# Performance work log

Hardware: AMD Instinct MI355X
Metric: run time of the kernel (lower is better)

Reference implementation:

```python
import jax, jax.numpy as jnp
import numpy as np

NUM_HEADS = 12


def setup_inputs() -> dict:
    key = jax.random.key(0)
    ks = jax.random.split(key, 10)
    B, S, H = 4, 1024, 768
    hd = H // NUM_HEADS
    hk = hv = 64
    scale = 1.0 / np.sqrt(H)
    inp = {
        "hidden_states": jax.random.normal(ks[0], (B, S, H), dtype=jnp.float32),
        "attention_mask": jnp.ones((B, S), dtype=jnp.float32),
        "Wq": jax.random.normal(ks[1], (H, H), dtype=jnp.float32) * scale,
        "bq": jnp.zeros((H,), dtype=jnp.float32),
        "Wk": jax.random.normal(ks[2], (H, H), dtype=jnp.float32) * scale,
        "bk": jnp.zeros((H,), dtype=jnp.float32),
        "Wv": jax.random.normal(ks[3], (H, H), dtype=jnp.float32) * scale,
        "bv": jnp.zeros((H,), dtype=jnp.float32),
        "E_key": jax.random.normal(ks[4], (2 * hk + 1, hd), dtype=jnp.float32) * 0.02,
        "E_val": jax.random.normal(ks[5], (2 * hv + 1, hd), dtype=jnp.float32) * 0.02,
    }
    return inp


def reference(hidden_states, attention_mask, Wq, bq, Wk, bk, Wv, bv, E_key, E_val):
    B, S, H = hidden_states.shape
    hd = H // NUM_HEADS

    def split_heads(x):  # [B,S,H] -> [B,nh,S,hd]
        return x.reshape(B, S, NUM_HEADS, hd).transpose(0, 2, 1, 3)

    q = split_heads(hidden_states @ Wq + bq)
    k = split_heads(hidden_states @ Wk + bk)
    v = split_heads(hidden_states @ Wv + bv)

    # content scores (note: original code applies NO 1/sqrt(d) scaling)
    scores = jnp.einsum("bhid,bhjd->bhij", q, k)

    # relative key-position scores: scores_pos[i,j] = q_i . E_key[j-i+hk] (banded)
    Rk = E_key.shape[0]
    hk = (Rk - 1) // 2
    rel = jnp.arange(S)[None, :] - jnp.arange(S)[:, None] + hk  # [S,S]
    valid_k = (rel >= 0) & (rel < Rk)
    p = jnp.einsum("bhid,rd->bhir", q, E_key)  # [B,nh,S,Rk]
    rel_c = jnp.clip(rel, 0, Rk - 1)
    scores_pos = jnp.take_along_axis(p, rel_c[None, None, :, :], axis=-1)
    scores = scores + jnp.where(valid_k[None, None], scores_pos, 0.0)

    # attention mask: (1 - m) * finfo.min added to scores
    ext = (1.0 - attention_mask[:, None, None, :]) * jnp.finfo(scores.dtype).min
    probs = jax.nn.softmax(scores + ext, axis=-1)

    ctx = jnp.einsum("bhij,bhjd->bhid", probs, v)

    # relative value-position: ctx_pos[i] = sum_j probs[i,j] * E_val[j-i+hv]
    Rv = E_val.shape[0]
    hv = (Rv - 1) // 2
    j_idx = jnp.arange(S)[:, None] + jnp.arange(Rv)[None, :] - hv  # [S,Rv]
    valid_v = (j_idx >= 0) & (j_idx < S)
    j_c = jnp.clip(j_idx, 0, S - 1)
    probs_band = jnp.take_along_axis(probs, j_c[None, None, :, :], axis=-1)
    probs_band = probs_band * valid_v[None, None].astype(probs.dtype)
    ctx = ctx + jnp.einsum("bhir,rd->bhid", probs_band, E_val)

    return ctx.transpose(0, 2, 1, 3).reshape(B, S, H)
```

## Files before the change

### kernel.cpp

```cpp
#include <hip/hip_runtime.h>
#include <hip/hip_bf16.h>
#include <math.h>

#define NH 12
#define SEQ 1024
#define HD 64
#define HDIM 768
#define BSZ 4
#define RK 129
#define FMIN -3.4028234663852886e38f

typedef __attribute__((ext_vector_type(8))) short short8;
typedef __attribute__((ext_vector_type(4))) short short4v;
typedef __attribute__((ext_vector_type(8))) _Float16 f16x8;
typedef __attribute__((ext_vector_type(4))) float f32x4;

__device__ inline short f2bf(float x) {
    union { __hip_bfloat16 h; short s; } u;
    u.h = __float2bfloat16(x);
    return u.s;
}
__device__ inline float bf2f(short s) {
    union { __hip_bfloat16 h; short t; } u;
    u.t = s;
    return __bfloat162float(u.h);
}

__device__ inline void async_load16(void* lds, const void* g) {
    __builtin_amdgcn_global_load_lds(
        (const __attribute__((address_space(1))) unsigned int*)g,
        (__attribute__((address_space(3))) unsigned int*)lds, 16, 0, 0);
}

#define BAR()    asm volatile("s_barrier" ::: "memory")
#define WAITV0() asm volatile("s_waitcnt vmcnt(0)" ::: "memory")

#define NXCHUNK 393216
#define NECHUNK 1032
#define NEVCHUNK 1280
#define NCONVB ((NXCHUNK + NECHUNK + NEVCHUNK + 255) / 256)
#define NTRB   (144 * 3)
__global__ __launch_bounds__(256) void prep_kernel(
    const float* __restrict__ X, const float* __restrict__ Ek,
    const float* __restrict__ Ev,
    const float* __restrict__ Wq, const float* __restrict__ Wk, const float* __restrict__ Wv,
    _Float16* __restrict__ Xh, _Float16* __restrict__ Ekh, short* __restrict__ Evt,
    _Float16* __restrict__ Wtq, _Float16* __restrict__ Wtk, _Float16* __restrict__ Wtv)
{
    const int bidg = blockIdx.x;
    if (bidg < NCONVB) {
        int idx = bidg * 256 + threadIdx.x;
        if (idx < NXCHUNK + NECHUNK) {
            const float* src;
            _Float16* dst;
            if (idx < NXCHUNK) { src = X; dst = Xh; }
            else { idx -= NXCHUNK; src = Ek; dst = Ekh; }
            float4 a = ((const float4*)src)[idx * 2];
            float4 b = ((const float4*)src)[idx * 2 + 1];
            f16x8 o;
            o[0] = (_Float16)a.x; o[1] = (_Float16)a.y; o[2] = (_Float16)a.z; o[3] = (_Float16)a.w;
            o[4] = (_Float16)b.x; o[5] = (_Float16)b.y; o[6] = (_Float16)b.z; o[7] = (_Float16)b.w;
            ((f16x8*)dst)[idx] = o;
        } else if (idx < NXCHUNK + NECHUNK + NEVCHUNK) {
            idx -= NXCHUNK + NECHUNK;
            const int dim = idx / 20;
            const int r0  = (idx % 20) * 8;
            short8 o;
#pragma unroll
            for (int e = 0; e < 8; ++e) {
                int rel = r0 + e;
                float v = (rel < RK) ? Ev[(size_t)rel * HD + dim] : 0.0f;
                o[e] = f2bf(v);
            }
            *(short8*)&Evt[(size_t)dim * 160 + r0] = o;
        }
        return;
    }
    const int bid2 = bidg - NCONVB;
    const int z = bid2 / 144;
    const int r = bid2 % 144;
    const float* __restrict__ W = (z == 0) ? Wq : (z == 1) ? Wk : Wv;
    _Float16* __restrict__ Wt   = (z == 0) ? Wtq : (z == 1) ? Wtk : Wtv;

    __shared__ float sT[64][65];
    const int t  = threadIdx.x;
    const int k0 = (r / 12) * 64;
    const int n0 = (r % 12) * 64;

    const int c  = (t & 15) * 4;
    const int kr = t >> 4;
#pragma unroll
    for (int rr = 0; rr < 4; ++rr) {
        float4 v = *(const float4*)&W[(size_t)(k0 + kr + rr * 16) * HDIM + n0 + c];
        sT[c + 0][kr + rr * 16] = v.x;
        sT[c + 1][kr + rr * 16] = v.y;
        sT[c + 2][kr + rr * 16] = v.z;
        sT[c + 3][kr + rr * 16] = v.w;
    }
    __syncthreads();
    const int rn = t >> 2;
    const int ck = (t & 3) * 16;
#pragma unroll
    for (int g = 0; g < 2; ++g) {
        f16x8 o;
#pragma unroll
        for (int e = 0; e < 8; ++e) o[e] = (_Float16)sT[rn][ck + g * 8 + e];
        *(f16x8*)&Wt[(size_t)(n0 + rn) * HDIM + k0 + ck + g * 8] = o;
    }
}

__global__ __launch_bounds__(256) void qkv_mfma_kernel(
    const _Float16* __restrict__ Xh,
    const _Float16* __restrict__ Wtq, const _Float16* __restrict__ Wtk, const _Float16* __restrict__ Wtv,
    const float* __restrict__ bq, const float* __restrict__ bk, const float* __restrict__ bv,
    _Float16* __restrict__ Qo, _Float16* __restrict__ Ko, short* __restrict__ Vt)
{
    int bid = blockIdx.x;
    bid = (bid & 7) * 72 + (bid >> 3);
    const int which = bid / 192;
    const int rem   = bid % 192;
    const int n0    = (rem / 32) * 128;
    const int m0    = (rem % 32) * 128;
    const _Float16* __restrict__ Wt = (which == 0) ? Wtq : (which == 1) ? Wtk : Wtv;
    const float* __restrict__ bias  = (which == 0) ? bq : (which == 1) ? bk : bv;

    __shared__ __align__(16) _Float16 sA[128 * 64];
    __shared__ __align__(16) _Float16 sB[128 * 64];

    const int t  = threadIdx.x;
    const int w  = t >> 6, l = t & 63;
    const int lq = l & 15, lg = l >> 4;
    const int wr = w >> 1, wc = w & 1;

    f32x4 acc[4][4];
#pragma unroll
    for (int i = 0; i < 4; ++i)
#pragma unroll
        for (int j = 0; j < 4; ++j) acc[i][j] = (f32x4){0.f, 0.f, 0.f, 0.f};

    for (int k0 = 0; k0 < HDIM; k0 += 64) {
        __syncthreads();
#pragma unroll
        for (int r = 0; r < 4; ++r) {
            const int cib = r * 256 + w * 64;
            const int ci  = cib + l;
            const int row = ci >> 3, cr = ci & 7;
            const int lc  = cr ^ (row & 7);
            async_load16(&sA[(size_t)cib * 8],
                         &Xh[(size_t)(m0 + row) * HDIM + k0 + lc * 8]);
            async_load16(&sB[(size_t)cib * 8],
                         &Wt[(size_t)(n0 + row) * HDIM + k0 + lc * 8]);
        }
        __syncthreads();

        f16x8 af[4][2], bf[4][2];
#pragma unroll
        for (int i = 0; i < 4; ++i) {
#pragma unroll
            for (int ks = 0; ks < 2; ++ks) {
                int ra = wr * 64 + i * 16 + lq;
                af[i][ks] = *(const f16x8*)((const char*)sA +
                            ra * 128 + ((ks * 64 + lg * 16) ^ ((ra & 7) << 4)));
                int rb = wc * 64 + i * 16 + lq;
                bf[i][ks] = *(const f16x8*)((const char*)sB +
                            rb * 128 + ((ks * 64 + lg * 16) ^ ((rb & 7) << 4)));
            }
        }
#pragma unroll
        for (int i = 0; i < 4; ++i)
#pragma unroll
            for (int j = 0; j < 4; ++j) {
                acc[i][j] = __builtin_amdgcn_mfma_f32_16x16x32_f16(af[i][0], bf[j][0], acc[i][j], 0, 0, 0);
                acc[i][j] = __builtin_amdgcn_mfma_f32_16x16x32_f16(af[i][1], bf[j][1], acc[i][j], 0, 0, 0);
            }
    }

    _Float16* __restrict__ Yh = (which == 0) ? Qo : Ko;
#pragma unroll
    for (int i = 0; i < 4; ++i) {
        const int mb = m0 + wr * 64 + i * 16 + lg * 4;
        const int bb = mb >> 10, ss = mb & 1023;
#pragma unroll
        for (int j = 0; j < 4; ++j) {
            const int n  = n0 + wc * 64 + j * 16 + lq;
            const float bv4 = bias[n];
            const int hh = n >> 6, dd = n & 63;
            if (which == 2) {
                short4v pk;
#pragma unroll
                for (int reg = 0; reg < 4; ++reg)
                    pk[reg] = f2bf(acc[i][j][reg] + bv4);
                *(short4v*)&Vt[((size_t)(bb * NH + hh) * HD + dd) * SEQ + ss] = pk;
            } else {
#pragma unroll
                for (int reg = 0; reg < 4; ++reg) {
                    const size_t off = ((size_t)(bb * NH + hh) * SEQ + ss + reg) * HD + dd;
                    Yh[off] = (_Float16)(acc[i][j][reg] + bv4);
                }
            }
        }
    }
}

__global__ __launch_bounds__(256, 2) void attn_mfma_kernel(
    const _Float16* __restrict__ Q, const _Float16* __restrict__ K,
    const short* __restrict__ Vt, const float* __restrict__ mask,
    const _Float16* __restrict__ Ekh, const short* __restrict__ Evt,
    float* __restrict__ out)
{
    __shared__ __align__(16) _Float16 sK[2][64][64];
    __shared__ __align__(16) short    sVT[2][64][64];
    __shared__ __align__(16) short    sPscr[4][16][64];
    __shared__ __align__(16) _Float16 sPpos[4][16][129];
    __shared__ __align__(16) short    sBand[4][16][160];
    __shared__ __align__(16) short    sMask[1024];

    int bid = blockIdx.x;
    bid = (bid & 7) * 96 + (bid >> 3);
    const int bh = bid >> 4;
    const int i0 = (bid & 15) * 64;
    const int b  = bh / NH;
    const int h  = bh - b * NH;

    const int t  = threadIdx.x;
    const int w  = t >> 6;
    const int l  = t & 63;
    const int lq = l & 15;
    const int lg = l >> 4;
    const int wrow0 = i0 + w * 16;

    {
        short8 z8 = {0, 0, 0, 0, 0, 0, 0, 0};
        short8* p = (short8*)&sBand[w][0][0];
        for (int idx = l; idx < 320; idx += 64) p[idx] = z8;
    }
#pragma unroll
    for (int r = 0; r < 2; ++r) {
        const int ci = r * 256 + w * 64 + l;
        const int row = ci >> 3;
        const int lc  = (ci & 7) ^ (row & 7);
        async_load16((char*)sK + ci * 16,
                     K + ((size_t)bh * SEQ + row) * HD + lc * 8);
        async_load16((char*)sVT + ci * 16,
                     Vt + ((size_t)bh * HD + row) * SEQ + lc * 8);
    }

    const _Float16* qp = Q + ((size_t)bh * SEQ + wrow0 + lq) * HD;
    f16x8 qf0 = *(const f16x8*)&qp[lg * 8];
    f16x8 qf1 = *(const f16x8*)&qp[32 + lg * 8];

#pragma unroll
    for (int nt = 0; nt < 9; ++nt) {
        int cc = nt * 16 + lq;
        f16x8 eb0 = {0, 0, 0, 0, 0, 0, 0, 0};
        f16x8 eb1 = {0, 0, 0, 0, 0, 0, 0, 0};
        if (cc < RK) {
            eb0 = *(const f16x8*)&Ekh[(size_t)cc * HD + lg * 8];
            eb1 = *(const f16x8*)&Ekh[(size_t)cc * HD + 32 + lg * 8];
        }
        f32x4 pc = {0.f, 0.f, 0.f, 0.f};
        pc = __builtin_amdgcn_mfma_f32_16x16x32_f16(qf0, eb0, pc, 0, 0, 0);
        pc = __builtin_amdgcn_mfma_f32_16x16x32_f16(qf1, eb1, pc, 0, 0, 0);
        if (cc < RK) {
#pragma unroll
            for (int reg = 0; reg < 4; ++reg)
                sPpos[w][lg * 4 + reg][cc] = (_Float16)pc[reg];
        }
    }

    {
        float4 mv = *(const float4*)&mask[(size_t)b * SEQ + t * 4];
        short4v mo;
        mo[0] = f2bf((1.0f - mv.x) * FMIN);
        mo[1] = f2bf((1.0f - mv.y) * FMIN);
        mo[2] = f2bf((1.0f - mv.z) * FMIN);
        mo[3] = f2bf((1.0f - mv.w) * FMIN);
        *(short4v*)&sMask[t * 4] = mo;
    }

    asm volatile("s_waitcnt vmcnt(0) lgkmcnt(0)" ::: "memory");
    BAR();

    f32x4 acc[4];
#pragma unroll
    for (int nt = 0; nt < 4; ++nt) acc[nt] = (f32x4){0.f, 0.f, 0.f, 0.f};
    float lacc[4] = {0.f, 0.f, 0.f, 0.f};

    const int ck0 = lg ^ (lq & 7);
    const int ck1 = (4 + lg) ^ (lq & 7);
    short* sPw = &sPscr[w][0][0];

    for (int jt = 0; jt < 16; ++jt) {
        const int cur = jt & 1;
        const int j0  = jt * 64;

        if (jt < 15) {
            const int jn0 = j0 + 64;
#pragma unroll
            for (int r = 0; r < 2; ++r) {
                const int ci = r * 256 + w * 64 + l;
                const int row = ci >> 3;
                const int lc  = (ci & 7) ^ (row & 7);
                async_load16((char*)sK + (cur ^ 1) * 8192 + ci * 16,
                             K + ((size_t)bh * SEQ + jn0 + row) * HD + lc * 8);
                async_load16((char*)sVT + (cur ^ 1) * 8192 + ci * 16,
                             Vt + ((size_t)bh * HD + row) * SEQ + jn0 + lc * 8);
            }
        }

        const char* sKc = (const char*)sK + cur * 8192;
        f32x4 sc[4];
#pragma unroll
        for (int ct = 0; ct < 4; ++ct) {
            const int rb = (ct * 16 + lq) * 128;
            f16x8 kb0 = *(const f16x8*)(sKc + rb + ck0 * 16);
            f16x8 kb1 = *(const f16x8*)(sKc + rb + ck1 * 16);
            f32x4 s = {0.f, 0.f, 0.f, 0.f};
            s = __builtin_amdgcn_mfma_f32_16x16x32_f16(qf0, kb0, s, 0, 0, 0);
            s = __builtin_amdgcn_mfma_f32_16x16x32_f16(qf1, kb1, s, 0, 0, 0);
            sc[ct] = s;
        }

        float mt[4];
#pragma unroll
        for (int ct = 0; ct < 4; ++ct) mt[ct] = bf2f(sMask[j0 + ct * 16 + lq]);

        const bool band_active = (j0 >= wrow0 - 127) && (j0 <= wrow0 + 79);
        if (band_active) {
#pragma unroll
            for (int ct = 0; ct < 4; ++ct) {
                const int relb = j0 + ct * 16 + lq - wrow0 - lg * 4 + 64;
#pragma unroll
                for (int reg = 0; reg < 4; ++reg) {
                    const int row = lg * 4 + reg;
                    const int rel = relb - reg;
                    float s = sc[ct][reg] + mt[ct];
                    const bool inb = ((unsigned)rel < (unsigned)RK);
                    if (inb) s += (float)sPpos[w][row][rel];
                    const float p = __expf(s);
                    lacc[reg] += p;
                    const short pb = f2bf(p);
                    sPw[row * 64 + ((ct * 16 + lq) ^ ((row & 7) << 3))] = pb;
                    if (inb) sBand[w][row][rel] = pb;
                }
            }
        } else {
#pragma unroll
            for (int ct = 0; ct < 4; ++ct) {
#pragma unroll
                for (int reg = 0; reg < 4; ++reg) {
                    const int row = lg * 4 + reg;
                    const float p = __expf(sc[ct][reg] + mt[ct]);
                    lacc[reg] += p;
                    sPw[row * 64 + ((ct * 16 + lq) ^ ((row & 7) << 3))] = f2bf(p);
                }
            }
        }

        short8 pa0 = *(const short8*)((const char*)sPw + lq * 128 + ck0 * 16);
        short8 pa1 = *(const short8*)((const char*)sPw + lq * 128 + ck1 * 16);
        const char* sVc = (const char*)sVT + cur * 8192;
#pragma unroll
        for (int nt = 0; nt < 4; ++nt) {
            const int rb = (nt * 16 + lq) * 128;
            short8 vb0 = *(const short8*)(sVc + rb + ck0 * 16);
            short8 vb1 = *(const short8*)(sVc + rb + ck1 * 16);
            acc[nt] = __builtin_amdgcn_mfma_f32_16x16x32_bf16(pa0, vb0, acc[nt], 0, 0, 0);
            acc[nt] = __builtin_amdgcn_mfma_f32_16x16x32_bf16(pa1, vb1, acc[nt], 0, 0, 0);
        }

        WAITV0();
        BAR();
    }

    float linv[4];
#pragma unroll
    for (int reg = 0; reg < 4; ++reg) {
        float lr = lacc[reg];
        lr += __shfl_xor(lr, 1);
        lr += __shfl_xor(lr, 2);
        lr += __shfl_xor(lr, 4);
        lr += __shfl_xor(lr, 8);
        linv[reg] = 1.0f / lr;
    }

    short8 bandA[5];
#pragma unroll
    for (int ks = 0; ks < 5; ++ks)
        bandA[ks] = *(const short8*)&sBand[w][lq][ks * 32 + lg * 8];
#pragma unroll
    for (int nt = 0; nt < 4; ++nt) {
#pragma unroll
        for (int ks = 0; ks < 5; ++ks) {
            short8 eb = *(const short8*)&Evt[(size_t)(nt * 16 + lq) * 160 + ks * 32 + lg * 8];
            acc[nt] = __builtin_amdgcn_mfma_f32_16x16x32_bf16(bandA[ks], eb, acc[nt], 0, 0, 0);
        }
    }

#pragma unroll
    for (int nt = 0; nt < 4; ++nt) {
#pragma unroll
        for (int reg = 0; reg < 4; ++reg) {
            int qi = wrow0 + lg * 4 + reg;
            out[((size_t)b * SEQ + qi) * HDIM + h * HD + nt * 16 + lq] =
                acc[nt][reg] * linv[reg];
        }
    }
}

extern "C" void kernel_launch(void* const* d_in, const int* in_sizes, int n_in,
                              void* d_out, int out_size, void* d_ws, size_t ws_size,
                              hipStream_t stream) {
    const float* X    = (const float*)d_in[0];
    const float* mask = (const float*)d_in[1];
    const float* Wq   = (const float*)d_in[2];
    const float* bq   = (const float*)d_in[3];
    const float* Wk   = (const float*)d_in[4];
    const float* bk   = (const float*)d_in[5];
    const float* Wv   = (const float*)d_in[6];
    const float* bv   = (const float*)d_in[7];
    const float* Ek   = (const float*)d_in[8];
    const float* Ev   = (const float*)d_in[9];
    float* out        = (float*)d_out;

    char* ws = (char*)d_ws;
    const size_t SZ_QKV = (size_t)BSZ * NH * SEQ * HD * 2;
    const size_t SZ_W   = (size_t)HDIM * HDIM * 2;
    _Float16* Qh  = (_Float16*)(ws);
    _Float16* Kh  = (_Float16*)(ws + SZ_QKV);
    short*    Vt  = (short*)   (ws + 2 * SZ_QKV);
    _Float16* Xh  = (_Float16*)(ws + 3 * SZ_QKV);
    _Float16* Wtq = (_Float16*)(ws + 4 * SZ_QKV);
    _Float16* Wtk = (_Float16*)(ws + 4 * SZ_QKV + SZ_W);
    _Float16* Wtv = (_Float16*)(ws + 4 * SZ_QKV + 2 * SZ_W);
    _Float16* Ekh = (_Float16*)(ws + 4 * SZ_QKV + 3 * SZ_W);
    short*    Evt = (short*)   (ws + 4 * SZ_QKV + 3 * SZ_W + 20480);

    prep_kernel<<<NCONVB + NTRB, 256, 0, stream>>>(
        X, Ek, Ev, Wq, Wk, Wv, Xh, Ekh, Evt, Wtq, Wtk, Wtv);
    qkv_mfma_kernel<<<576, 256, 0, stream>>>(Xh, Wtq, Wtk, Wtv, bq, bk, bv, Qh, Kh, Vt);
    attn_mfma_kernel<<<768, 256, 0, stream>>>(Qh, Kh, Vt, mask, Ekh, Evt, out);
}
```

Baseline: 88.98 us.

## Fold attention mask into V and compute softmax denominator via MFMA

The additive mask is turned into a multiplicative factor exp(mask), which is applied to V in the QKV epilogue and to the band probabilities. The row sum of exp(scores) is computed by an extra MFMA against the mask-factor vector instead of per-element accumulation and shuffle reductions. The QK MFMA operands are swapped so each lane holds a transposed score tile, which allows packed 32-bit stores of P to LDS. This removes per-element mask adds and the scalar denominator accumulation, but masked positions now become 0 times exp(score) rather than an exp underflow, which can overflow or give NaN if a score is large.

```diff
diff --git a/kernel.cpp b/kernel.cpp
--- a/kernel.cpp
+++ b/kernel.cpp
@@ -113,6 +113,7 @@
     const _Float16* __restrict__ Xh,
     const _Float16* __restrict__ Wtq, const _Float16* __restrict__ Wtk, const _Float16* __restrict__ Wtv,
     const float* __restrict__ bq, const float* __restrict__ bk, const float* __restrict__ bv,
+    const float* __restrict__ maskg,
     _Float16* __restrict__ Qo, _Float16* __restrict__ Ko, short* __restrict__ Vt)
 {
     int bid = blockIdx.x;
@@ -180,6 +181,14 @@
     for (int i = 0; i < 4; ++i) {
         const int mb = m0 + wr * 64 + i * 16 + lg * 4;
         const int bb = mb >> 10, ss = mb & 1023;
+        float zz[4] = {1.f, 1.f, 1.f, 1.f};
+        if (which == 2) {
+            float4 mv = *(const float4*)&maskg[(size_t)bb * SEQ + ss];
+            zz[0] = __expf((1.0f - mv.x) * FMIN);
+            zz[1] = __expf((1.0f - mv.y) * FMIN);
+            zz[2] = __expf((1.0f - mv.z) * FMIN);
+            zz[3] = __expf((1.0f - mv.w) * FMIN);
+        }
 #pragma unroll
         for (int j = 0; j < 4; ++j) {
             const int n  = n0 + wc * 64 + j * 16 + lq;
@@ -189,7 +198,7 @@
                 short4v pk;
 #pragma unroll
                 for (int reg = 0; reg < 4; ++reg)
-                    pk[reg] = f2bf(acc[i][j][reg] + bv4);
+                    pk[reg] = f2bf((acc[i][j][reg] + bv4) * zz[reg]);
                 *(short4v*)&Vt[((size_t)(bb * NH + hh) * HD + dd) * SEQ + ss] = pk;
             } else {
 #pragma unroll
@@ -213,7 +222,7 @@
     __shared__ __align__(16) short    sPscr[4][16][64];
     __shared__ __align__(16) _Float16 sPpos[4][16][129];
     __shared__ __align__(16) short    sBand[4][16][160];
-    __shared__ __align__(16) short    sMask[1024];
+    __shared__ __align__(16) short    sZ[1024];
 
     int bid = blockIdx.x;
     bid = (bid & 7) * 96 + (bid >> 3);
@@ -270,12 +279,12 @@
 
     {
         float4 mv = *(const float4*)&mask[(size_t)b * SEQ + t * 4];
-        short4v mo;
-        mo[0] = f2bf((1.0f - mv.x) * FMIN);
-        mo[1] = f2bf((1.0f - mv.y) * FMIN);
-        mo[2] = f2bf((1.0f - mv.z) * FMIN);
-        mo[3] = f2bf((1.0f - mv.w) * FMIN);
-        *(short4v*)&sMask[t * 4] = mo;
+        short4v zo;
+        zo[0] = f2bf(__expf((1.0f - mv.x) * FMIN));
+        zo[1] = f2bf(__expf((1.0f - mv.y) * FMIN));
+        zo[2] = f2bf(__expf((1.0f - mv.z) * FMIN));
+        zo[3] = f2bf(__expf((1.0f - mv.w) * FMIN));
+        *(short4v*)&sZ[t * 4] = zo;
     }
 
     asm volatile("s_waitcnt vmcnt(0) lgkmcnt(0)" ::: "memory");
@@ -284,11 +293,12 @@
     f32x4 acc[4];
 #pragma unroll
     for (int nt = 0; nt < 4; ++nt) acc[nt] = (f32x4){0.f, 0.f, 0.f, 0.f};
-    float lacc[4] = {0.f, 0.f, 0.f, 0.f};
+    f32x4 zacc = {0.f, 0.f, 0.f, 0.f};
 
     const int ck0 = lg ^ (lq & 7);
     const int ck1 = (4 + lg) ^ (lq & 7);
-    short* sPw = &sPscr[w][0][0];
+    char* sPw = (char*)&sPscr[w][0][0];
+    const int swz = (lq & 7) << 4;
 
     for (int jt = 0; jt < 16; ++jt) {
         const int cur = jt & 1;
@@ -316,49 +326,56 @@
             f16x8 kb0 = *(const f16x8*)(sKc + rb + ck0 * 16);
             f16x8 kb1 = *(const f16x8*)(sKc + rb + ck1 * 16);
             f32x4 s = {0.f, 0.f, 0.f, 0.f};
-            s = __builtin_amdgcn_mfma_f32_16x16x32_f16(qf0, kb0, s, 0, 0, 0);
-            s = __builtin_amdgcn_mfma_f32_16x16x32_f16(qf1, kb1, s, 0, 0, 0);
+            s = __builtin_amdgcn_mfma_f32_16x16x32_f16(kb0, qf0, s, 0, 0, 0);
+            s = __builtin_amdgcn_mfma_f32_16x16x32_f16(kb1, qf1, s, 0, 0, 0);
             sc[ct] = s;
         }
 
-        float mt[4];
-#pragma unroll
-        for (int ct = 0; ct < 4; ++ct) mt[ct] = bf2f(sMask[j0 + ct * 16 + lq]);
-
+        float p[4][4];
         const bool band_active = (j0 >= wrow0 - 127) && (j0 <= wrow0 + 79);
         if (band_active) {
 #pragma unroll
             for (int ct = 0; ct < 4; ++ct) {
-                const int relb = j0 + ct * 16 + lq - wrow0 - lg * 4 + 64;
+                const int kbase = j0 + ct * 16 + lg * 4;
+                const int relb  = kbase - wrow0 - lq + 64;
+                short4v zv4 = *(const short4v*)&sZ[kbase];
 #pragma unroll
                 for (int reg = 0; reg < 4; ++reg) {
-                    const int row = lg * 4 + reg;
-                    const int rel = relb - reg;
-                    float s = sc[ct][reg] + mt[ct];
+                    float s = sc[ct][reg];
+                    const int rel = relb + reg;
                     const bool inb = ((unsigned)rel < (unsigned)RK);
-                    if (inb) s += (float)sPpos[w][row][rel];
-                    const float p = __expf(s);
-                    lacc[reg] += p;
-                    const short pb = f2bf(p);
-                    sPw[row * 64 + ((ct * 16 + lq) ^ ((row & 7) << 3))] = pb;
-                    if (inb) sBand[w][row][rel] = pb;
+                    if (inb) s += (float)sPpos[w][lq][rel];
+                    const float pv = __expf(s);
+                    p[ct][reg] = pv;
+                    if (inb) sBand[w][lq][rel] = f2bf(pv * bf2f(zv4[reg]));
                 }
             }
         } else {
 #pragma unroll
-            for (int ct = 0; ct < 4; ++ct) {
-#pragma unroll
-                for (int reg = 0; reg < 4; ++reg) {
-                    const int row = lg * 4 + reg;
-                    const float p = __expf(sc[ct][reg] + mt[ct]);
-                    lacc[reg] += p;
-                    sPw[row * 64 + ((ct * 16 + lq) ^ ((row & 7) << 3))] = f2bf(p);
-                }
-            }
-        }
-
-        short8 pa0 = *(const short8*)((const char*)sPw + lq * 128 + ck0 * 16);
-        short8 pa1 = *(const short8*)((const char*)sPw + lq * 128 + ck1 * 16);
+            for (int ct = 0; ct < 4; ++ct)
+#pragma unroll
+                for (int reg = 0; reg < 4; ++reg)
+                    p[ct][reg] = __expf(sc[ct][reg]);
+        }
+
+#pragma unroll
+        for (int ct = 0; ct < 4; ++ct)
+#pragma unroll
+            for (int hh = 0; hh < 2; ++hh) {
+                unsigned pw =
+                    (unsigned short)f2bf(p[ct][2 * hh]) |
+                    ((unsigned)(unsigned short)f2bf(p[ct][2 * hh + 1]) << 16);
+                *(unsigned*)(sPw + lq * 128 +
+                             ((ct * 32 + lg * 8 + hh * 4) ^ swz)) = pw;
+            }
+
+        short8 pa0 = *(const short8*)(sPw + lq * 128 + ((lg * 16) ^ swz));
+        short8 pa1 = *(const short8*)(sPw + lq * 128 + ((64 + lg * 16) ^ swz));
+        short8 zb0 = *(const short8*)&sZ[j0 + lg * 8];
+        short8 zb1 = *(const short8*)&sZ[j0 + 32 + lg * 8];
+        zacc = __builtin_amdgcn_mfma_f32_16x16x32_bf16(pa0, zb0, zacc, 0, 0, 0);
+        zacc = __builtin_amdgcn_mfma_f32_16x16x32_bf16(pa1, zb1, zacc, 0, 0, 0);
+
         const char* sVc = (const char*)sVT + cur * 8192;
 #pragma unroll
         for (int nt = 0; nt < 4; ++nt) {
@@ -373,17 +390,6 @@
         BAR();
     }
 
-    float linv[4];
-#pragma unroll
-    for (int reg = 0; reg < 4; ++reg) {
-        float lr = lacc[reg];
-        lr += __shfl_xor(lr, 1);
-        lr += __shfl_xor(lr, 2);
-        lr += __shfl_xor(lr, 4);
-        lr += __shfl_xor(lr, 8);
-        linv[reg] = 1.0f / lr;
-    }
-
     short8 bandA[5];
 #pragma unroll
     for (int ks = 0; ks < 5; ++ks)
@@ -403,7 +409,7 @@
         for (int reg = 0; reg < 4; ++reg) {
             int qi = wrow0 + lg * 4 + reg;
             out[((size_t)b * SEQ + qi) * HDIM + h * HD + nt * 16 + lq] =
-                acc[nt][reg] * linv[reg];
+                acc[nt][reg] / zacc[reg];
         }
     }
 }
@@ -438,6 +444,6 @@
 
     prep_kernel<<<NCONVB + NTRB, 256, 0, stream>>>(
         X, Ek, Ev, Wq, Wk, Wv, Xh, Ekh, Evt, Wtq, Wtk, Wtv);
-    qkv_mfma_kernel<<<576, 256, 0, stream>>>(Xh, Wtq, Wtk, Wtv, bq, bk, bv, Qh, Kh, Vt);
+    qkv_mfma_kernel<<<576, 256, 0, stream>>>(Xh, Wtq, Wtk, Wtv, bq, bk, bv, mask, Qh, Kh, Vt);
     attn_mfma_kernel<<<768, 256, 0, stream>>>(Qh, Kh, Vt, mask, Ekh, Evt, out);
 }
```

Result: slower. 103.4 us (+16.2%).
